# Optimization experiments

Hardware: AMD Instinct MI355X
Metric: run time of the kernel (lower is better)

The kernel has to match this reference:

```python
import jax, jax.numpy as jnp
import numpy as np

B, H, G, N, D = 1, 32, 64, 128, 128   # batch, heads, blocks, block_len, head_dim
S = 256                               # sketch dim (multiple of 16)
BIT_PACK = 8


def setup_inputs() -> dict:
    key = jax.random.key(0)
    k1, k2, k3 = jax.random.split(key, 3)
    data = jax.random.normal(k1, (B, H, G, N, D), dtype=jnp.float32)
    # binary per-channel outlier mask, float {0,1}, shape matches data.shape[:3] + (D,)
    outlier_mask = jax.random.randint(k2, (B, H, G, D), 0, 2).astype(jnp.float32)
    # proj_dir_quant = proj_dir_score.T -> shape (S, D)
    proj_dir_quant = jax.random.normal(k3, (S, D), dtype=jnp.float32)
    return {"data": data, "outlier_mask": outlier_mask, "proj_dir_quant": proj_dir_quant}


def _pack_bits(sketch):
    # sketch: (..., S). Reshape to (..., S//8, 8), threshold at 0, pack sign bits into uint8.
    x = sketch.reshape(*sketch.shape[:-1], -1, BIT_PACK)
    enc = (2 ** jnp.arange(BIT_PACK, dtype=jnp.int32))  # [1,2,4,...,128]
    packed = ((x > 0).astype(jnp.int32) * enc).sum(axis=-1)  # max 255, fits uint8
    return packed.astype(jnp.uint8)


def reference(data, outlier_mask, proj_dir_quant):
    s = proj_dir_quant.shape[0]
    m = outlier_mask[..., None, :]                     # (B,H,G,1,D) broadcast over tokens
    key_outlier = data * m
    key_inlier = data * (1.0 - m)
    # '...nd,sd->...ns' : sign-random-projection sketch
    sk_outlier = jnp.einsum('bhgnd,sd->bhgns', key_outlier, proj_dir_quant)
    sk_inlier = jnp.einsum('bhgnd,sd->bhgns', key_inlier, proj_dir_quant)
    hash_inlier = _pack_bits(sk_inlier)                # (B,H,G,N,S//8)
    hash_outlier = _pack_bits(sk_outlier)[..., : s // 16]  # (B,H,G,N,S//16)
    return (hash_inlier, hash_outlier)
```

## Files before the change

### kernel.cpp

```cpp
#include <hip/hip_runtime.h>

#define NB_HG 2048
#define DIM_N 128
#define DIM_D 128
#define DIM_S 256
#define PH 32
#define BSW 128


__global__ void transpose_proj_kernel(const float* __restrict__ proj,
                                      float* __restrict__ projT)
{
    const int d = blockIdx.x;
    const int s = threadIdx.x;
    projT[d * DIM_S + s] = proj[s * DIM_D + d];
}

template<bool TP>
__global__ __launch_bounds__(256)
void qjl_sketch_kernel(const float* __restrict__ data,
                       const float* __restrict__ mask,
                       const float* __restrict__ pmat,
                       int* __restrict__ out)
{
    __shared__ float Xt[PH * DIM_N];
    __shared__ float Bs[PH * BSW];
    __shared__ int   cidx[DIM_D];
    __shared__ int   wcnt[2];

    const int type = blockIdx.x;
    const int hg   = blockIdx.y;
    const int tid  = threadIdx.x;

    bool sel = false; int pos = 0, w = 0;
    if (tid < 128) {
        const float m = mask[hg * DIM_D + tid];
        sel = (type == 2) ? (m != 0.0f) : (m == 0.0f);
        const unsigned long long bal = __ballot(sel);
        const int lane = tid & 63;
        w = tid >> 6;
        if (lane == 0) wcnt[w] = __popcll(bal);
        pos = __popcll(bal & ((1ull << lane) - 1ull));
    }
    __syncthreads();
    if (sel) cidx[pos + (w ? wcnt[0] : 0)] = tid;
    __syncthreads();
    const int K = wcnt[0] + wcnt[1];

    const int tn = tid & 15;
    const int ts = tid >> 4;
    const int C0 = 4 * tn;
    const int sl = ts * 8;
    const int sbase = (type == 1) ? 128 : 0;

    float acc[8][8];
    #pragma unroll
    for (int j = 0; j < 8; ++j)
        #pragma unroll
        for (int i = 0; i < 8; ++i) acc[j][i] = 0.0f;

    const int cl_s  = tid & 31;
    const int nh    = tid >> 5;
    const int pcs_s = 4 * (cl_s & 7);
    float* xrow = &Xt[cl_s * DIM_N];
    float* brow = &Bs[cl_s * BSW];

    auto STAGE = [&](int base, int kp) {
        if (cl_s < kp) {
            const int dg = cidx[base + cl_s];
            const float* Xs = data + (size_t)hg * (DIM_N * DIM_D) + dg;
            #pragma unroll
            for (int g = 0; g < 4; ++g) {
                const int n0 = nh * 16 + g * 4;
                float4 v;
                v.x = Xs[(size_t)(n0 + 0) * DIM_D];
                v.y = Xs[(size_t)(n0 + 1) * DIM_D];
                v.z = Xs[(size_t)(n0 + 2) * DIM_D];
                v.w = Xs[(size_t)(n0 + 3) * DIM_D];
                *reinterpret_cast<float4*>(&xrow[n0 ^ pcs_s]) = v;
            }
            if (TP) {
                const float* Ps = pmat + (size_t)dg * DIM_S + sbase;
                #pragma unroll
                for (int g = 0; g < 4; ++g) {
                    const int s0l = nh * 16 + g * 4;
                    const float4 b = *reinterpret_cast<const float4*>(Ps + s0l);
                    *reinterpret_cast<float4*>(&brow[s0l ^ pcs_s]) = b;
                }
            } else {
                #pragma unroll
                for (int g = 0; g < 4; ++g) {
                    const int s0l = nh * 16 + g * 4;
                    float4 b;
                    b.x = pmat[(size_t)(sbase + s0l + 0) * DIM_D + dg];
                    b.y = pmat[(size_t)(sbase + s0l + 1) * DIM_D + dg];
                    b.z = pmat[(size_t)(sbase + s0l + 2) * DIM_D + dg];
                    b.w = pmat[(size_t)(sbase + s0l + 3) * DIM_D + dg];
                    *reinterpret_cast<float4*>(&brow[s0l ^ pcs_s]) = b;
                }
            }
        }
    };

    auto COMPUTE = [&](int kp) {
        #pragma unroll 8
        for (int cl = 0; cl < kp; ++cl) {
            const int pcs = 4 * (cl & 7);
            const int pA  = sl ^ pcs;
            const float4 bA = *reinterpret_cast<const float4*>(&Bs[cl * BSW + pA]);
            const float4 bB = *reinterpret_cast<const float4*>(&Bs[cl * BSW + (pA ^ 4)]);
            const int P = C0 ^ pcs;
            const float4 q0 = *reinterpret_cast<const float4*>(&Xt[cl * DIM_N + P]);
            const float4 q1 = *reinterpret_cast<const float4*>(&Xt[cl * DIM_N + P + 64]);
            const float bv[8] = {bA.x, bA.y, bA.z, bA.w, bB.x, bB.y, bB.z, bB.w};

            #pragma unroll
            for (int j = 0; j < 8; ++j) {
                acc[j][0] = fmaf(bv[j], q0.x, acc[j][0]);
                acc[j][1] = fmaf(bv[j], q0.y, acc[j][1]);
                acc[j][2] = fmaf(bv[j], q0.z, acc[j][2]);
                acc[j][3] = fmaf(bv[j], q0.w, acc[j][3]);
                acc[j][4] = fmaf(bv[j], q1.x, acc[j][4]);
                acc[j][5] = fmaf(bv[j], q1.y, acc[j][5]);
                acc[j][6] = fmaf(bv[j], q1.z, acc[j][6]);
                acc[j][7] = fmaf(bv[j], q1.w, acc[j][7]);
            }
        }
    };

    for (int base = 0; base < K; base += PH) {
        const int kp = (K - base < PH) ? (K - base) : PH;
        if (base) __syncthreads();
        STAGE(base, kp);
        __syncthreads();
        COMPUTE(kp);
    }

    const size_t inl_total = (size_t)NB_HG * DIM_N * 32;
    #pragma unroll
    for (int i = 0; i < 8; ++i) {
        int byte = 0;
        #pragma unroll
        for (int j = 0; j < 8; ++j)
            if (acc[j][i] > 0.0f) byte |= (1 << j);
        const int n = (i < 4) ? (C0 + i) : (64 + C0 + (i - 4));
        size_t idx;
        if (type == 2)
            idx = inl_total + ((size_t)hg * DIM_N + n) * 16 + ts;
        else
            idx = ((size_t)hg * DIM_N + n) * 32 + (type == 1 ? 16 : 0) + ts;
        out[idx] = byte;
    }
}

extern "C" void kernel_launch(void* const* d_in, const int* in_sizes, int n_in,
                              void* d_out, int out_size, void* d_ws, size_t ws_size,
                              hipStream_t stream) {
    const float* data = (const float*)d_in[0];
    const float* mask = (const float*)d_in[1];
    const float* proj = (const float*)d_in[2];
    int* out = (int*)d_out;

    dim3 grid(3, NB_HG);
    const size_t tp_bytes = (size_t)DIM_D * DIM_S * sizeof(float);
    if (ws_size >= tp_bytes) {
        float* projT = (float*)d_ws;
        transpose_proj_kernel<<<DIM_D, DIM_S, 0, stream>>>(proj, projT);
        qjl_sketch_kernel<true><<<grid, 256, 0, stream>>>(data, mask, projT, out);
    } else {
        qjl_sketch_kernel<false><<<grid, 256, 0, stream>>>(data, mask, proj, out);
    }
}
```

Baseline: 187.9 us.

## Prefetch next K-chunk into registers while computing current chunk

Splits the staging step into a global-to-register load and a register-to-shared write. The next chunk's global loads are issued before computing on the current chunk, so their latency overlaps with the FMA loop. This adds 32 live registers per thread, which may reduce occupancy, and keeps the same number of barriers per chunk.

```diff
diff --git a/kernel.cpp b/kernel.cpp
--- a/kernel.cpp
+++ b/kernel.cpp
@@ -65,39 +65,44 @@
     float* xrow = &Xt[cl_s * DIM_N];
     float* brow = &Bs[cl_s * BSW];
 
-    auto STAGE = [&](int base, int kp) {
+    float4 xr[4], br[4];
+
+    auto LOADR = [&](int base, int kp) {
         if (cl_s < kp) {
             const int dg = cidx[base + cl_s];
             const float* Xs = data + (size_t)hg * (DIM_N * DIM_D) + dg;
             #pragma unroll
             for (int g = 0; g < 4; ++g) {
                 const int n0 = nh * 16 + g * 4;
-                float4 v;
-                v.x = Xs[(size_t)(n0 + 0) * DIM_D];
-                v.y = Xs[(size_t)(n0 + 1) * DIM_D];
-                v.z = Xs[(size_t)(n0 + 2) * DIM_D];
-                v.w = Xs[(size_t)(n0 + 3) * DIM_D];
-                *reinterpret_cast<float4*>(&xrow[n0 ^ pcs_s]) = v;
+                xr[g].x = Xs[(size_t)(n0 + 0) * DIM_D];
+                xr[g].y = Xs[(size_t)(n0 + 1) * DIM_D];
+                xr[g].z = Xs[(size_t)(n0 + 2) * DIM_D];
+                xr[g].w = Xs[(size_t)(n0 + 3) * DIM_D];
             }
             if (TP) {
                 const float* Ps = pmat + (size_t)dg * DIM_S + sbase;
                 #pragma unroll
-                for (int g = 0; g < 4; ++g) {
-                    const int s0l = nh * 16 + g * 4;
-                    const float4 b = *reinterpret_cast<const float4*>(Ps + s0l);
-                    *reinterpret_cast<float4*>(&brow[s0l ^ pcs_s]) = b;
-                }
+                for (int g = 0; g < 4; ++g)
+                    br[g] = *reinterpret_cast<const float4*>(Ps + nh * 16 + g * 4);
             } else {
                 #pragma unroll
                 for (int g = 0; g < 4; ++g) {
                     const int s0l = nh * 16 + g * 4;
-                    float4 b;
-                    b.x = pmat[(size_t)(sbase + s0l + 0) * DIM_D + dg];
-                    b.y = pmat[(size_t)(sbase + s0l + 1) * DIM_D + dg];
-                    b.z = pmat[(size_t)(sbase + s0l + 2) * DIM_D + dg];
-                    b.w = pmat[(size_t)(sbase + s0l + 3) * DIM_D + dg];
-                    *reinterpret_cast<float4*>(&brow[s0l ^ pcs_s]) = b;
+                    br[g].x = pmat[(size_t)(sbase + s0l + 0) * DIM_D + dg];
+                    br[g].y = pmat[(size_t)(sbase + s0l + 1) * DIM_D + dg];
+                    br[g].z = pmat[(size_t)(sbase + s0l + 2) * DIM_D + dg];
+                    br[g].w = pmat[(size_t)(sbase + s0l + 3) * DIM_D + dg];
                 }
+            }
+        }
+    };
+    auto WRITER = [&](int kp) {
+        if (cl_s < kp) {
+            #pragma unroll
+            for (int g = 0; g < 4; ++g) {
+                const int n0 = nh * 16 + g * 4;
+                *reinterpret_cast<float4*>(&xrow[n0 ^ pcs_s]) = xr[g];
+                *reinterpret_cast<float4*>(&brow[n0 ^ pcs_s]) = br[g];
             }
         }
     };
@@ -128,12 +133,23 @@
         }
     };
 
+    {
+        const int kp0 = (K < PH) ? K : PH;
+        LOADR(0, kp0);
+        WRITER(kp0);
+        __syncthreads();
+    }
     for (int base = 0; base < K; base += PH) {
-        const int kp = (K - base < PH) ? (K - base) : PH;
-        if (base) __syncthreads();
-        STAGE(base, kp);
-        __syncthreads();
-        COMPUTE(kp);
+        const int kpc = (K - base < PH) ? (K - base) : PH;
+        const int nb  = base + PH;
+        const int kpn = (nb < K) ? ((K - nb < PH) ? (K - nb) : PH) : 0;
+        if (kpn) LOADR(nb, kpn);
+        COMPUTE(kpc);
+        if (kpn) {
+            __syncthreads();
+            WRITER(kpn);
+            __syncthreads();
+        }
     }
 
     const size_t inl_total = (size_t)NB_HG * DIM_N * 32;
```

Measured after the change: 215.6 us. 1.15x slower.
